# Optimization experiments

Measured on AMD Instinct MI355X. Metric: run time of the kernel, lower is better.

## Reference

```python
import jax, jax.numpy as jnp
import numpy as np

N_NODES, N_EDGES = 10000, 100000
NODE_DIM, NUM_BASIS = 128, 20
MULS = {0: 128, 1: 64, 2: 32}            # 128x0e + 64x1e + 32x2e
NUM_IRREPS = 224                          # total multiplicity count
HIDDEN = NODE_DIM + NUM_IRREPS            # 352
SPH_DIM = 128 * 1 + 64 * 3 + 32 * 5       # 480
LN_EPS = 1e-5

def _s2_basis():
    # orthonormal (Frobenius) basis of symmetric traceless 3x3 matrices (real l=2)
    s = np.zeros((5, 3, 3)); r2 = 1.0 / np.sqrt(2.0)
    s[0, 0, 1] = s[0, 1, 0] = r2
    s[1, 1, 2] = s[1, 2, 1] = r2
    s[2] = np.diag([-1.0, -1.0, 2.0]) / np.sqrt(6.0)
    s[3, 0, 2] = s[3, 2, 0] = r2
    s[4] = np.diag([1.0, -1.0, 0.0]) * r2
    return s

def _cg_tables():
    # real Clebsch-Gordan tensors for l<=2 built from the invariant tensors
    # delta, Levi-Civita, and the symmetric-traceless basis; unit Frobenius norm (e3nn w3j convention)
    e3 = np.zeros((3, 3, 3))
    e3[0, 1, 2] = e3[1, 2, 0] = e3[2, 0, 1] = 1.0
    e3[0, 2, 1] = e3[2, 1, 0] = e3[1, 0, 2] = -1.0
    S = _s2_basis(); I3 = np.eye(3); I5 = np.eye(5)
    nrm = lambda c: (c / np.linalg.norm(c)).astype(np.float32)
    cg = {(0, 0, 0): np.ones((1, 1, 1), np.float32)}
    cg[(0, 1, 1)] = nrm(I3[None]); cg[(1, 0, 1)] = nrm(I3[:, None, :]); cg[(1, 1, 0)] = nrm(I3[:, :, None])
    cg[(0, 2, 2)] = nrm(I5[None]); cg[(2, 0, 2)] = nrm(I5[:, None, :]); cg[(2, 2, 0)] = nrm(I5[:, :, None])
    cg[(1, 1, 1)] = nrm(e3)
    cg[(1, 1, 2)] = nrm(np.transpose(S, (1, 2, 0)))
    cg[(1, 2, 1)] = nrm(np.transpose(S, (1, 0, 2)))
    cg[(2, 1, 1)] = nrm(S)
    cg[(2, 2, 1)] = nrm(np.einsum('ijk,Mil,Nlj->MNk', e3, S, S))
    cg[(1, 2, 2)] = nrm(np.einsum('iab,Mac,Ncb->iMN', e3, S, S))
    cg[(2, 1, 2)] = nrm(np.einsum('jab,Mac,Ncb->MjN', e3, S, S))
    cg[(2, 2, 2)] = nrm(np.einsum('Mab,Nbc,Pca->MNP', S, S, S))
    return cg

CG = _cg_tables()
PATHS = [(0, 0, 0), (1, 1, 0), (2, 2, 0),
         (0, 1, 1), (1, 0, 1), (1, 1, 1), (1, 2, 1), (2, 1, 1), (2, 2, 1),
         (0, 2, 2), (1, 1, 2), (1, 2, 2), (2, 0, 2), (2, 1, 2), (2, 2, 2)]
FAN = {0: 224, 1: 384, 2: 352}   # e3nn 'element' path-norm fan-in per output irrep
TP_NUMW = sum(MULS[l1] * MULS[l3] for (l1, _, l3) in PATHS)

def _layernorm(x, w, b):
    mu = x.mean(-1, keepdims=True)
    var = ((x - mu) ** 2).mean(-1, keepdims=True)
    return (x - mu) * jax.lax.rsqrt(var + LN_EPS) * w + b

def _o3_layernorm(x, w, b):
    # equivariant layer norm: per-irrep RMS over (mul, m); mean-centering + bias only for scalars
    n = x.shape[0]; outs = []; off = 0; woff = 0
    for l in (0, 1, 2):
        mul, d = MULS[l], 2 * l + 1
        f = x[:, off:off + mul * d].reshape(n, mul, d)
        if l == 0:
            f = f - f.mean(axis=1, keepdims=True)
        nrm = (f * f).mean(axis=(1, 2), keepdims=True)
        f = f * jax.lax.rsqrt(nrm + LN_EPS) * w[woff:woff + mul][None, :, None]
        if l == 0:
            f = f + b[None, :, None]
        outs.append(f.reshape(n, mul * d)); off += mul * d; woff += mul
    return jnp.concatenate(outs, -1)

def _fc_tp(x1, x2, tp_w):
    # FullyConnectedTensorProduct(128x0e+64x1e+32x2e, 1x0e+1x1e+1x2e -> 128x0e+64x1e+32x2e)
    outs = {0: 0.0, 1: 0.0, 2: 0.0}; off = 0
    for (l1, l2, l3) in PATHS:
        m1, m3 = MULS[l1], MULS[l3]
        W = tp_w[off:off + m1 * m3].reshape(m1, m3); off += m1 * m3
        pw = float(np.sqrt((2 * l3 + 1) / FAN[l3]))
        outs[l3] = outs[l3] + pw * jnp.einsum('eum,en,mnk,uw->ewk', x1[l1], x2[l2], jnp.asarray(CG[(l1, l2, l3)]), W, optimize=True)
    e = x2[0].shape[0]
    return jnp.concatenate([outs[l].reshape(e, -1) for l in (0, 1, 2)], -1)

def _forward(x_scalar, x_spherical, rbf, rsh, ln_w, ln_b, o3_w, o3_b,
             mlp_w1, mlp_b1, mlp_w2, mlp_b2, rbf_w, tp_w, edge_index):
    scalar_in = _layernorm(x_scalar, ln_w, ln_b)                # [N,128]
    spherical_in = _o3_layernorm(x_spherical, o3_w, o3_b)       # [N,480]
    h = jax.nn.silu(scalar_in @ mlp_w1 + mlp_b1)
    scalar_out = h @ mlp_w2 + mlp_b2                            # [N,352]
    filt = rbf @ rbf_w                                          # [E,352]
    dst, src = edge_index[0], edge_index[1]
    fo = scalar_out[src] * filt                                 # gather + RBF filter
    gate, msg_scalar = fo[:, :NUM_IRREPS], fo[:, NUM_IRREPS:]
    sph = spherical_in[src]                                     # [E,480]
    e = sph.shape[0]
    # ElementwiseTensorProduct(edge_irreps, 224x0e): per-channel scalar gating
    x1 = {0: (sph[:, :128] * gate[:, :128])[:, :, None],
          1: sph[:, 128:320].reshape(e, 64, 3) * gate[:, 128:192, None],
          2: sph[:, 320:480].reshape(e, 32, 5) * gate[:, 192:224, None]}
    x2 = {0: rsh[:, :1], 1: rsh[:, 1:4], 2: rsh[:, 4:9]}
    msg_sph = _fc_tp(x1, x2, tp_w)                              # [E,480]
    new_scalar = scalar_in.at[dst].add(msg_scalar)
    new_spherical = spherical_in.at[dst].add(msg_sph)
    return new_scalar, new_spherical

def setup_inputs():
    key = jax.random.key(0)
    ks = jax.random.split(key, 9)
    return {
        'x_scalar': jax.random.normal(ks[0], (N_NODES, NODE_DIM), jnp.float32),
        'x_spherical': jax.random.normal(ks[1], (N_NODES, SPH_DIM), jnp.float32),
        'rbf': jax.random.uniform(ks[2], (N_EDGES, NUM_BASIS), jnp.float32),
        'rsh': jax.random.normal(ks[3], (N_EDGES, 9), jnp.float32),
        'edge_index': jax.random.randint(ks[4], (2, N_EDGES), 0, N_NODES, dtype=jnp.int32),
        'ln_w': jnp.ones((NODE_DIM,), jnp.float32),
        'ln_b': jnp.zeros((NODE_DIM,), jnp.float32),
        'o3_w': jnp.ones((NUM_IRREPS,), jnp.float32),
        'o3_b': jnp.zeros((128,), jnp.float32),
        'mlp_w1': jax.random.normal(ks[5], (NODE_DIM, NODE_DIM), jnp.float32) / np.sqrt(NODE_DIM),
        'mlp_b1': jnp.zeros((NODE_DIM,), jnp.float32),
        'mlp_w2': jax.random.normal(ks[6], (NODE_DIM, HIDDEN), jnp.float32) / np.sqrt(NODE_DIM),
        'mlp_b2': jnp.zeros((HIDDEN,), jnp.float32),
        'rbf_w': jax.random.normal(ks[7], (NUM_BASIS, HIDDEN), jnp.float32) / np.sqrt(NUM_BASIS),
        'tp_w': jax.random.normal(ks[8], (TP_NUMW,), jnp.float32),
    }

def reference(x_scalar, x_spherical, rbf, rsh, edge_index, ln_w, ln_b, o3_w, o3_b,
              mlp_w1, mlp_b1, mlp_w2, mlp_b2, rbf_w, tp_w):
    return _forward(x_scalar, x_spherical, rbf, rsh, ln_w, ln_b, o3_w, o3_b,
                    mlp_w1, mlp_b1, mlp_w2, mlp_b2, rbf_w, tp_w, edge_index)
```

## Files before the change

### kernel.cpp

```cpp
#include <hip/hip_runtime.h>

#define NN 10000
#define NE 100000
#define ND 128
#define NB 20
#define NIR 224
#define NH 352
#define SD 480
#define BS 512

#define CR   0.70710678118654752f
#define CA   0.40824829046386302f
#define HA   0.20412414523193151f
#define HR   0.35355339059327376f
#define C110 0.57735026918962576f
#define C220 0.44721359549995794f
#define C111 0.40824829046386302f
#define C11X 0.44721359549995794f
#define C221 0.36514837167011074f
#define C222 0.58554004376912270f
#define S32  0.86602540378443865f
#define PW0  0.066815310478106094f
#define PW1  0.088388347648318447f
#define PW2  0.11918321088232916f

typedef __bf16 v8bf __attribute__((ext_vector_type(8)));
typedef unsigned short us8v __attribute__((ext_vector_type(8)));
typedef float f32x4 __attribute__((ext_vector_type(4)));

__device__ __forceinline__ unsigned short f2bfc(float f) {
  __bf16 h = (__bf16)f;
  return __builtin_bit_cast(unsigned short, h);
}
__device__ __forceinline__ float bf2f(unsigned short h) {
  unsigned int u = ((unsigned int)h) << 16;
  return __builtin_bit_cast(float, u);
}

__device__ __forceinline__ float warpReduceSum(float v) {
  #pragma unroll
  for (int off = 32; off > 0; off >>= 1) v += __shfl_down(v, off, 64);
  return v;
}

__global__ __launch_bounds__(128) void node_ln_kernel(
    const float* __restrict__ xs, const float* __restrict__ xsph,
    const float* __restrict__ lnw, const float* __restrict__ lnb,
    const float* __restrict__ o3w, const float* __restrict__ o3b,
    float* __restrict__ s_in, float* __restrict__ sph_in,
    float* __restrict__ out0)
{
  const int n = blockIdx.x, t = threadIdx.x;
  __shared__ float red[4];

  auto reduce2 = [&](float a, float b) {
    a = warpReduceSum(a); b = warpReduceSum(b);
    if ((t & 63) == 0) { red[(t >> 6) * 2] = a; red[(t >> 6) * 2 + 1] = b; }
    __syncthreads();
    float ra = red[0] + red[2], rb = red[1] + red[3];
    __syncthreads();
    return make_float2(ra, rb);
  };

  float x = xs[n * ND + t];
  float2 sr = reduce2(x, x * x);
  float mu = sr.x * (1.f / ND);
  float var = sr.y * (1.f / ND) - mu * mu;
  float y = (x - mu) * rsqrtf(var + 1e-5f) * lnw[t] + lnb[t];
  s_in[n * ND + t] = y; out0[n * ND + t] = y;

  float f = xsph[n * SD + t];
  float2 r0 = reduce2(f, f * f);
  float m0 = r0.x * (1.f / 128.f);
  float nrm0 = r0.y * (1.f / 128.f) - m0 * m0;
  float y0 = (f - m0) * rsqrtf(nrm0 + 1e-5f) * o3w[t] + o3b[t];
  sph_in[n * SD + t] = y0;

  float f1a = xsph[n * SD + 128 + t];
  float f1b = (t < 64) ? xsph[n * SD + 256 + t] : 0.f;
  float2 r1 = reduce2(f1a * f1a + f1b * f1b, 0.f);
  float rs1 = rsqrtf(r1.x * (1.f / 192.f) + 1e-5f);
  sph_in[n * SD + 128 + t] = f1a * rs1 * o3w[128 + t / 3];
  if (t < 64)
    sph_in[n * SD + 256 + t] = f1b * rs1 * o3w[128 + (128 + t) / 3];

  float f2a = xsph[n * SD + 320 + t];
  float f2b = (t < 32) ? xsph[n * SD + 448 + t] : 0.f;
  float2 r2 = reduce2(f2a * f2a + f2b * f2b, 0.f);
  float rs2 = rsqrtf(r2.x * (1.f / 160.f) + 1e-5f);
  sph_in[n * SD + 320 + t] = f2a * rs2 * o3w[192 + t / 5];
  if (t < 32)
    sph_in[n * SD + 448 + t] = f2b * rs2 * o3w[192 + (128 + t) / 5];
}

#define NPB 8
__global__ __launch_bounds__(256) void mlp_kernel(
    const float* __restrict__ s_in, const float* __restrict__ w1,
    const float* __restrict__ b1, const float* __restrict__ w2,
    const float* __restrict__ b2, float* __restrict__ s_out)
{
  __shared__ float sIn[NPB][ND];
  __shared__ float sH[NPB][ND];
  const int t = threadIdx.x;
  const int n0 = blockIdx.x * NPB;
  for (int i = t; i < NPB * ND; i += 256) sIn[i >> 7][i & 127] = s_in[n0 * ND + i];
  __syncthreads();
  {
    const int j = t & 127, g = t >> 7;
    float acc[4] = {0.f, 0.f, 0.f, 0.f};
    for (int k = 0; k < ND; ++k) {
      float w = w1[k * ND + j];
      #pragma unroll
      for (int i = 0; i < 4; ++i) acc[i] = fmaf(sIn[g + 2 * i][k], w, acc[i]);
    }
    #pragma unroll
    for (int i = 0; i < 4; ++i) {
      float z = acc[i] + b1[j];
      sH[g + 2 * i][j] = z / (1.f + __expf(-z));
    }
  }
  __syncthreads();
  for (int jb = 0; jb < 2; ++jb) {
    int j = jb * 256 + t;
    if (j < NH) {
      float acc[NPB];
      #pragma unroll
      for (int i = 0; i < NPB; ++i) acc[i] = b2[j];
      for (int k = 0; k < ND; ++k) {
        float w = w2[k * NH + j];
        #pragma unroll
        for (int i = 0; i < NPB; ++i) acc[i] = fmaf(sH[i][k], w, acc[i]);
      }
      #pragma unroll
      for (int i = 0; i < NPB; ++i) s_out[(n0 + i) * NH + j] = acc[i];
    }
  }
}

__device__ __forceinline__ float wc0(const float* w, int u, int j) {
  int off = (u < 128) ? u * 128 : (u < 192) ? 16384 + (u - 128) * 128 : 24576 + (u - 192) * 128;
  return w[off + j];
}
__device__ __forceinline__ float wc1(const float* w, int u, int j) {
  int off = (u < 128) ? 28672 + u * 64 : (u < 192) ? 36864 + (u - 128) * 64
          : (u < 256) ? 40960 + (u - 192) * 64 : (u < 320) ? 45056 + (u - 256) * 64
          : (u < 352) ? 49152 + (u - 320) * 64 : 51200 + (u - 352) * 64;
  return w[off + j];
}
__device__ __forceinline__ float wc2(const float* w, int u, int j) {
  int off = (u < 128) ? 53248 + u * 32 : (u < 192) ? 57344 + (u - 128) * 32
          : (u < 256) ? 59392 + (u - 192) * 32 : (u < 288) ? 61440 + (u - 256) * 32
          : (u < 320) ? 62464 + (u - 288) * 32 : 63488 + (u - 320) * 32;
  return w[off + j];
}

__global__ __launch_bounds__(256) void prep_w_kernel(
    const float* __restrict__ tpw, const float* __restrict__ rbf_w,
    unsigned short* __restrict__ W0g, unsigned short* __restrict__ W1g,
    unsigned short* __restrict__ W2g, unsigned short* __restrict__ Wfq)
{
  int gid = blockIdx.x * 256 + threadIdx.x;
  int i = gid & 7, lane = (gid >> 3) & 63;
  int r = lane & 15, kl = lane >> 4;
  if (gid < 28672) {
    int fid = gid >> 9, kk = fid >> 3, wid = fid & 7;
    W0g[gid] = f2bfc(wc0(tpw, kk * 32 + kl * 8 + i, wid * 16 + r));
  } else if (gid < 53248) {
    int g = gid - 28672, fid = g >> 9, kk = fid >> 2, nt = fid & 3;
    W1g[g] = f2bfc(wc1(tpw, kk * 32 + kl * 8 + i, nt * 16 + r));
  } else if (gid < 65536) {
    int g = gid - 53248, fid = g >> 9, q = fid >> 2, kh = (fid >> 1) & 1, ntc = fid & 1;
    int kk = kh * 6 + q;
    W2g[g] = (kk < 11) ? f2bfc(wc2(tpw, kk * 32 + kl * 8 + i, ntc * 16 + r)) : (unsigned short)0;
  } else if (gid < 90112) {
    int g = gid - 65536, fid = g >> 9, q = fid >> 3, wid = fid & 7;
    int t44 = wid + q * 8, nt = t44 >> 1, k = kl * 8 + i;
    Wfq[g] = (t44 < 44 && k < 20) ? f2bfc(rbf_w[k * NH + nt * 16 + r]) : (unsigned short)0;
  }
}

template<int M>
__device__ __forceinline__ void emit_dot(unsigned short* dst, const unsigned short* x1,
                                         const int* offs, const float* cf) {
  us8v xv[M];
  #pragma unroll
  for (int m = 0; m < M; ++m) xv[m] = *(const us8v*)&x1[offs[m]];
  v8bf o;
  #pragma unroll
  for (int i = 0; i < 8; ++i) {
    float a = 0.f;
    #pragma unroll
    for (int m = 0; m < M; ++m) a = fmaf(cf[m], bf2f(xv[m][i]), a);
    o[i] = (__bf16)a;
  }
  *(us8v*)dst = __builtin_bit_cast(us8v, o);
}

#define TSW(e, idx) ((idx) ^ (((e) & 7) << 3))

__device__ __forceinline__ void build0(unsigned short* Tb, const unsigned short* X1u,
                                       const float* RshF, int tid) {
  for (int it = tid; it < 32 * 28; it += BS) {
    int e = it / 28, ub = it - e * 28, u0 = ub * 8;
    const float* R = &RshF[e * 9];
    const unsigned short* x1 = &X1u[e * 480];
    unsigned short* dst = Tb + TSW(e, e * 384 + u0);
    if (u0 < 128) {
      float cf[1] = { PW0 * R[0] };
      int offs[1] = { u0 };
      emit_dot<1>(dst, x1, offs, cf);
    } else if (u0 < 192) {
      int m0 = u0 - 128;
      float cf[3] = { PW0 * C110 * R[1], PW0 * C110 * R[2], PW0 * C110 * R[3] };
      int offs[3] = { 128 + m0, 192 + m0, 256 + m0 };
      emit_dot<3>(dst, x1, offs, cf);
    } else {
      int m0 = u0 - 192;
      float cf[5] = { PW0 * C220 * R[4], PW0 * C220 * R[5], PW0 * C220 * R[6],
                      PW0 * C220 * R[7], PW0 * C220 * R[8] };
      int offs[5] = { 320 + m0, 352 + m0, 384 + m0, 416 + m0, 448 + m0 };
      emit_dot<5>(dst, x1, offs, cf);
    }
  }
}

template<int k>
__device__ __forceinline__ void build1(unsigned short* Tb, const unsigned short* X1u,
                                       const float* RshF, int tid) {
  for (int it = tid; it < 32 * 48; it += BS) {
    int e = it / 48, ub = it - e * 48, u0 = ub * 8;
    const float* R = &RshF[e * 9];
    const unsigned short* x1 = &X1u[e * 480];
    unsigned short* dst = Tb + TSW(e, e * 384 + u0);
    const float s = R[0], v0 = R[1], v1 = R[2], v2 = R[3];
    const float w0 = R[4], w1 = R[5], w2 = R[6], w3 = R[7], w4 = R[8];
    if (u0 < 128) {
      float cf[1] = { PW1 * C110 * R[1 + k] };
      int offs[1] = { u0 };
      emit_dot<1>(dst, x1, offs, cf);
    } else if (u0 < 192) {
      float cf[1] = { PW1 * C110 * s };
      int offs[1] = { 128 + k * 64 + (u0 - 128) };
      emit_dot<1>(dst, x1, offs, cf);
    } else if (u0 < 256) {
      constexpr int ka = (k + 1) % 3, kb = (k + 2) % 3;
      int m0 = u0 - 192;
      float cf[2] = { PW1 * C111 * R[1 + kb], -PW1 * C111 * R[1 + ka] };
      int offs[2] = { 128 + ka * 64 + m0, 128 + kb * 64 + m0 };
      emit_dot<2>(dst, x1, offs, cf);
    } else if (u0 < 320) {
      int m0 = u0 - 256;
      float cf[3];
      if constexpr (k == 0) { cf[0] = PW1*C11X*(-CA*w2 + CR*w4); cf[1] = PW1*C11X*CR*w0; cf[2] = PW1*C11X*CR*w3; }
      else if constexpr (k == 1) { cf[0] = PW1*C11X*CR*w0; cf[1] = PW1*C11X*(-CA*w2 - CR*w4); cf[2] = PW1*C11X*CR*w1; }
      else { cf[0] = PW1*C11X*CR*w3; cf[1] = PW1*C11X*CR*w1; cf[2] = PW1*C11X*2.f*CA*w2; }
      int offs[3] = { 128 + m0, 192 + m0, 256 + m0 };
      emit_dot<3>(dst, x1, offs, cf);
    } else if (u0 < 352) {
      int m0 = u0 - 320;
      if constexpr (k == 0) {
        float cf[4] = { PW1*C11X*CR*v1, PW1*C11X*(-CA*v0), PW1*C11X*CR*v2, PW1*C11X*CR*v0 };
        int offs[4] = { 320 + m0, 384 + m0, 416 + m0, 448 + m0 };
        emit_dot<4>(dst, x1, offs, cf);
      } else if constexpr (k == 1) {
        float cf[4] = { PW1*C11X*CR*v0, PW1*C11X*CR*v2, PW1*C11X*(-CA*v1), PW1*C11X*(-CR*v1) };
        int offs[4] = { 320 + m0, 352 + m0, 384 + m0, 448 + m0 };
        emit_dot<4>(dst, x1, offs, cf);
      } else {
        float cf[3] = { PW1*C11X*CR*v1, PW1*C11X*2.f*CA*v2, PW1*C11X*CR*v0 };
        int offs[3] = { 352 + m0, 384 + m0, 416 + m0 };
        emit_dot<3>(dst, x1, offs, cf);
      }
    } else {
      int m0 = u0 - 352;
      if constexpr (k == 0) {
        float cf[5] = { PW1*C221*0.5f*w3, PW1*C221*(S32*w2 + 0.5f*w4), PW1*C221*(-S32*w1),
                        PW1*C221*(-0.5f*w0), PW1*C221*(-0.5f*w1) };
        int offs[5] = { 320 + m0, 352 + m0, 384 + m0, 416 + m0, 448 + m0 };
        emit_dot<5>(dst, x1, offs, cf);
      } else if constexpr (k == 1) {
        float cf[5] = { PW1*C221*(-0.5f*w1), PW1*C221*0.5f*w0, PW1*C221*S32*w3,
                        PW1*C221*(-S32*w2 + 0.5f*w4), PW1*C221*(-0.5f*w3) };
        int offs[5] = { 320 + m0, 352 + m0, 384 + m0, 416 + m0, 448 + m0 };
        emit_dot<5>(dst, x1, offs, cf);
      } else {
        float cf[4] = { PW1*C221*(-w4), PW1*C221*(-0.5f*w3), PW1*C221*0.5f*w1, PW1*C221*w0 };
        int offs[4] = { 320 + m0, 352 + m0, 416 + m0, 448 + m0 };
        emit_dot<4>(dst, x1, offs, cf);
      }
    }
  }
}

template<int K>
__device__ __forceinline__ void build2(unsigned short* Tb, const unsigned short* X1u,
                                       const float* RshF, int tid) {
  for (int it = tid; it < 32 * 44; it += BS) {
    int e = it / 44, ub = it - e * 44, u0 = ub * 8;
    const float* R = &RshF[e * 9];
    const unsigned short* x1 = &X1u[e * 480];
    unsigned short* dst = Tb + TSW(e, e * 384 + u0);
    const float s = R[0], v0 = R[1], v1 = R[2], v2 = R[3];
    const float w0 = R[4], w1 = R[5], w2 = R[6], w3 = R[7], w4 = R[8];
    if (u0 < 128) {
      float cf[1] = { PW2 * C220 * R[4 + K] };
      int offs[1] = { u0 };
      emit_dot<1>(dst, x1, offs, cf);
    } else if (u0 < 192) {
      int m0 = u0 - 128;
      if constexpr (K == 0) {
        float cf[2] = { PW2*C11X*CR*v1, PW2*C11X*CR*v0 };
        int offs[2] = { 128 + m0, 192 + m0 };
        emit_dot<2>(dst, x1, offs, cf);
      } else if constexpr (K == 1) {
        float cf[2] = { PW2*C11X*CR*v2, PW2*C11X*CR*v1 };
        int offs[2] = { 192 + m0, 256 + m0 };
        emit_dot<2>(dst, x1, offs, cf);
      } else if constexpr (K == 2) {
        float cf[3] = { PW2*C11X*(-CA*v0), PW2*C11X*(-CA*v1), PW2*C11X*2.f*CA*v2 };
        int offs[3] = { 128 + m0, 192 + m0, 256 + m0 };
        emit_dot<3>(dst, x1, offs, cf);
      } else if constexpr (K == 3) {
        float cf[2] = { PW2*C11X*CR*v2, PW2*C11X*CR*v0 };
        int offs[2] = { 128 + m0, 256 + m0 };
        emit_dot<2>(dst, x1, offs, cf);
      } else {
        float cf[2] = { PW2*C11X*CR*v0, PW2*C11X*(-CR*v1) };
        int offs[2] = { 128 + m0, 192 + m0 };
        emit_dot<2>(dst, x1, offs, cf);
      }
    } else if (u0 < 256) {
      int m0 = u0 - 192;
      if constexpr (K == 2) {
        float cf[2] = { PW2*C221*S32*w1, PW2*C221*(-S32*w3) };
        int offs[2] = { 128 + m0, 192 + m0 };
        emit_dot<2>(dst, x1, offs, cf);
      } else {
        float cf[3];
        if constexpr (K == 0) { cf[0]=PW2*C221*(-0.5f*w3); cf[1]=PW2*C221*0.5f*w1; cf[2]=PW2*C221*w4; }
        else if constexpr (K == 1) { cf[0]=PW2*C221*(-S32*w2 - 0.5f*w4); cf[1]=PW2*C221*(-0.5f*w0); cf[2]=PW2*C221*0.5f*w3; }
        else if constexpr (K == 3) { cf[0]=PW2*C221*0.5f*w0; cf[1]=PW2*C221*(S32*w2 - 0.5f*w4); cf[2]=PW2*C221*(-0.5f*w1); }
        else { cf[0]=PW2*C221*0.5f*w1; cf[1]=PW2*C221*0.5f*w3; cf[2]=PW2*C221*(-w0); }
        int offs[3] = { 128 + m0, 192 + m0, 256 + m0 };
        emit_dot<3>(dst, x1, offs, cf);
      }
    } else if (u0 < 288) {
      int m0 = u0 - 256;
      float cf[1] = { PW2 * C220 * s };
      int offs[1] = { 320 + K * 32 + m0 };
      emit_dot<1>(dst, x1, offs, cf);
    } else if (u0 < 320) {
      int m0 = u0 - 288;
      if constexpr (K == 0) {
        float cf[3] = { PW2*C221*0.5f*v1, PW2*C221*(-0.5f*v0), PW2*C221*v2 };
        int offs[3] = { 352 + m0, 416 + m0, 448 + m0 };
        emit_dot<3>(dst, x1, offs, cf);
      } else if constexpr (K == 1) {
        float cf[4] = { PW2*C221*(-0.5f*v1), PW2*C221*(-S32*v0), PW2*C221*0.5f*v2, PW2*C221*(-0.5f*v0) };
        int offs[4] = { 320 + m0, 384 + m0, 416 + m0, 448 + m0 };
        emit_dot<4>(dst, x1, offs, cf);
      } else if constexpr (K == 2) {
        float cf[2] = { PW2*C221*S32*v0, PW2*C221*(-S32*v1) };
        int offs[2] = { 352 + m0, 416 + m0 };
        emit_dot<2>(dst, x1, offs, cf);
      } else if constexpr (K == 3) {
        float cf[4] = { PW2*C221*0.5f*v0, PW2*C221*(-0.5f*v2), PW2*C221*S32*v1, PW2*C221*(-0.5f*v1) };
        int offs[4] = { 320 + m0, 352 + m0, 384 + m0, 448 + m0 };
        emit_dot<4>(dst, x1, offs, cf);
      } else {
        float cf[3] = { PW2*C221*(-v2), PW2*C221*0.5f*v0, PW2*C221*0.5f*v1 };
        int offs[3] = { 320 + m0, 352 + m0, 416 + m0 };
        emit_dot<3>(dst, x1, offs, cf);
      }
    } else {
      int m0 = u0 - 320;
      if constexpr (K == 0) {
        float cf[4] = { PW2*C222*(-CA*w2), PW2*C222*HR*w3, PW2*C222*(-CA*w0), PW2*C222*HR*w1 };
        int offs[4] = { 320 + m0, 352 + m0, 384 + m0, 416 + m0 };
        emit_dot<4>(dst, x1, offs, cf);
      } else if constexpr (K == 4) {
        float cf[4] = { PW2*C222*(-HR*w1), PW2*C222*(-CA*w4), PW2*C222*HR*w3, PW2*C222*(-CA*w2) };
        int offs[4] = { 352 + m0, 384 + m0, 416 + m0, 448 + m0 };
        emit_dot<4>(dst, x1, offs, cf);
      } else {
        float cf[5];
        if constexpr (K == 1) { cf[0]=PW2*C222*HR*w3; cf[1]=PW2*C222*(HA*w2 - HR*w4); cf[2]=PW2*C222*HA*w1; cf[3]=PW2*C222*HR*w0; cf[4]=PW2*C222*(-HR*w1); }
        else if constexpr (K == 2) { cf[0]=PW2*C222*(-CA*w0); cf[1]=PW2*C222*HA*w1; cf[2]=PW2*C222*CA*w2; cf[3]=PW2*C222*HA*w3; cf[4]=PW2*C222*(-CA*w4); }
        else { cf[0]=PW2*C222*HR*w1; cf[1]=PW2*C222*HR*w0; cf[2]=PW2*C222*HA*w3; cf[3]=PW2*C222*(HA*w2 + HR*w4); cf[4]=PW2*C222*HR*w3; }
        int offs[5] = { 320 + m0, 352 + m0, 384 + m0, 416 + m0, 448 + m0 };
        emit_dot<5>(dst, x1, offs, cf);
      }
    }
  }
}

__global__ __launch_bounds__(BS, 4) void tp_fused_kernel(
    const float* __restrict__ rbf, const float* __restrict__ rsh,
    const int* __restrict__ ei, const float* __restrict__ s_out,
    const float* __restrict__ sph_in,
    const unsigned short* __restrict__ W0g, const unsigned short* __restrict__ W1g,
    const unsigned short* __restrict__ W2g, const unsigned short* __restrict__ Wfq,
    float* __restrict__ out0, float* __restrict__ out1T)
{
  __shared__ __align__(16) unsigned char smem[81280];
  unsigned short* Tb0 = (unsigned short*)smem;
  unsigned short* Tb1 = (unsigned short*)(smem + 24576);
  unsigned short* gateU = (unsigned short*)smem;
  unsigned short* rbfpadU = (unsigned short*)(smem + 24576);
  unsigned short* X1u = (unsigned short*)(smem + 49152);
  float* RshF = (float*)(smem + 79872);
  int* EdstS = (int*)(smem + 81024);
  int* EsrcS = (int*)(smem + 81152);

  const int tid = threadIdx.x;
  const int wid = tid >> 6, lane = tid & 63;
  const int r = lane & 15, kl = lane >> 4;

  auto MFMA = [](v8bf a, v8bf b, f32x4 c) {
    return __builtin_amdgcn_mfma_f32_16x16x32_bf16(a, b, c, 0, 0, 0);
  };
  auto ldw = [&](const unsigned short* base, int fid) {
    return __builtin_bit_cast(v8bf, *(const us8v*)&base[fid * 512 + lane * 8]);
  };

  auto mfma_l0 = [&](const unsigned short* T) {
    f32x4 acc0 = {0.f, 0.f, 0.f, 0.f}, acc1 = {0.f, 0.f, 0.f, 0.f};
    #pragma unroll
    for (int kk = 0; kk < 7; ++kk) {
      v8bf b = ldw(W0g, kk * 8 + wid);
      us8v a0 = *(const us8v*)&T[TSW(r, r * 384 + kl * 8 + kk * 32)];
      us8v a1 = *(const us8v*)&T[TSW(r, (16 + r) * 384 + kl * 8 + kk * 32)];
      acc0 = MFMA(__builtin_bit_cast(v8bf, a0), b, acc0);
      acc1 = MFMA(__builtin_bit_cast(v8bf, a1), b, acc1);
    }
    int col = wid * 16 + r;
    #pragma unroll
    for (int j = 0; j < 4; ++j) {
      unsafeAtomicAdd(&out1T[(long)EdstS[kl * 4 + j] * SD + col], acc0[j]);
      unsafeAtomicAdd(&out1T[(long)EdstS[16 + kl * 4 + j] * SD + col], acc1[j]);
    }
  };

  auto mfma_l1 = [&](const unsigned short* T, int k) {
    const int mt = wid >> 2, nt = wid & 3;
    f32x4 acc = {0.f, 0.f, 0.f, 0.f};
    #pragma unroll
    for (int kk = 0; kk < 12; ++kk) {
      v8bf b = ldw(W1g, kk * 4 + nt);
      us8v a = *(const us8v*)&T[TSW(r, (mt * 16 + r) * 384 + kl * 8 + kk * 32)];
      acc = MFMA(__builtin_bit_cast(v8bf, a), b, acc);
    }
    int col = 128 + k * 64 + nt * 16 + r;
    #pragma unroll
    for (int j = 0; j < 4; ++j)
      unsafeAtomicAdd(&out1T[(long)EdstS[mt * 16 + kl * 4 + j] * SD + col], acc[j]);
  };

  auto mfma_l2 = [&](const unsigned short* T, int K) {
    const int kh = wid >> 2, mt = (wid >> 1) & 1, ntc = wid & 1;
    f32x4 acc = {0.f, 0.f, 0.f, 0.f};
    #pragma unroll
    for (int q = 0; q < 6; ++q) {
      if (kh == 0 || q < 5) {
        v8bf b = ldw(W2g, q * 4 + kh * 2 + ntc);
        us8v a = *(const us8v*)&T[TSW(r, (mt * 16 + r) * 384 + kh * 192 + q * 32 + kl * 8)];
        acc = MFMA(__builtin_bit_cast(v8bf, a), b, acc);
      }
    }
    int col = 320 + K * 32 + ntc * 16 + r;
    #pragma unroll
    for (int j = 0; j < 4; ++j)
      unsafeAtomicAdd(&out1T[(long)EdstS[mt * 16 + kl * 4 + j] * SD + col], acc[j]);
  };

  for (int tile = blockIdx.x; tile < NE / 32; tile += gridDim.x) {
    const int e0 = tile * 32;
    for (int i = tid; i < 32; i += BS) { EdstS[i] = ei[e0 + i]; EsrcS[i] = ei[NE + e0 + i]; }
    for (int i = tid; i < 288; i += BS) RshF[i] = rsh[(long)e0 * 9 + i];
    for (int i = tid; i < 1024; i += BS) {
      int e = i >> 5, b = i & 31;
      rbfpadU[e * 40 + b] = (b < 20) ? f2bfc(rbf[(long)(e0 + e) * NB + b]) : (unsigned short)0;
    }
    __syncthreads();
    {
      us8v ra0 = *(const us8v*)&rbfpadU[r * 40 + kl * 8];
      us8v ra1 = *(const us8v*)&rbfpadU[(16 + r) * 40 + kl * 8];
      v8bf av0 = __builtin_bit_cast(v8bf, ra0);
      v8bf av1 = __builtin_bit_cast(v8bf, ra1);
      #pragma unroll
      for (int q = 0; q < 6; ++q) {
        int t44 = wid + q * 8;
        if (t44 < 44) {
          int mt = t44 & 1, nt = t44 >> 1;
          v8bf b = ldw(Wfq, q * 8 + wid);
          f32x4 acc = {0.f, 0.f, 0.f, 0.f};
          acc = MFMA(mt ? av1 : av0, b, acc);
          int gi = nt * 16 + r;
          #pragma unroll
          for (int j = 0; j < 4; ++j) {
            int e = mt * 16 + kl * 4 + j;
            float so = s_out[(long)EsrcS[e] * NH + gi];
            float val = acc[j] * so;
            if (nt < 14) gateU[e * 232 + gi] = f2bfc(val);
            else unsafeAtomicAdd(&out0[(long)EdstS[e] * ND + (gi - 224)], val);
          }
        }
      }
    }
    __syncthreads();
    for (int it = tid; it < 1920; it += BS) {
      int e = it / 60, cb = it - e * 60, c0 = cb * 8;
      long srow = (long)EsrcS[e] * SD;
      v8bf o;
      if (c0 < 128) {
        us8v gv = *(const us8v*)&gateU[e * 232 + c0];
        const float4 sa = *(const float4*)&sph_in[srow + c0];
        const float4 sb = *(const float4*)&sph_in[srow + c0 + 4];
        float sv[8] = {sa.x, sa.y, sa.z, sa.w, sb.x, sb.y, sb.z, sb.w};
        #pragma unroll
        for (int i = 0; i < 8; ++i) o[i] = (__bf16)(sv[i] * bf2f(gv[i]));
      } else if (c0 < 320) {
        int m = (c0 - 128) >> 6, mul0 = (c0 - 128) & 63;
        us8v gv = *(const us8v*)&gateU[e * 232 + 128 + mul0];
        #pragma unroll
        for (int i = 0; i < 8; ++i)
          o[i] = (__bf16)(sph_in[srow + 128 + (mul0 + i) * 3 + m] * bf2f(gv[i]));
      } else {
        int m = (c0 - 320) >> 5, mul0 = (c0 - 320) & 31;
        us8v gv = *(const us8v*)&gateU[e * 232 + 192 + mul0];
        #pragma unroll
        for (int i = 0; i < 8; ++i)
          o[i] = (__bf16)(sph_in[srow + 320 + (mul0 + i) * 5 + m] * bf2f(gv[i]));
      }
      *(us8v*)&X1u[e * 480 + c0] = __builtin_bit_cast(us8v, o);
    }
    __syncthreads();
    build0(Tb0, X1u, RshF, tid); __syncthreads();
    build1<0>(Tb1, X1u, RshF, tid); mfma_l0(Tb0); __syncthreads();
    build1<1>(Tb0, X1u, RshF, tid); mfma_l1(Tb1, 0); __syncthreads();
    build1<2>(Tb1, X1u, RshF, tid); mfma_l1(Tb0, 1); __syncthreads();
    build2<0>(Tb0, X1u, RshF, tid); mfma_l1(Tb1, 2); __syncthreads();
    build2<1>(Tb1, X1u, RshF, tid); mfma_l2(Tb0, 0); __syncthreads();
    build2<2>(Tb0, X1u, RshF, tid); mfma_l2(Tb1, 1); __syncthreads();
    build2<3>(Tb1, X1u, RshF, tid); mfma_l2(Tb0, 2); __syncthreads();
    build2<4>(Tb0, X1u, RshF, tid); mfma_l2(Tb1, 3); __syncthreads();
    mfma_l2(Tb0, 4); __syncthreads();
  }
}

__global__ __launch_bounds__(512) void merge_kernel(
    const float* __restrict__ sph_in, const float* __restrict__ out1T,
    float* __restrict__ out1)
{
  const int n = blockIdx.x, t = threadIdx.x;
  if (t < SD) {
    int tT;
    if (t < 128) tT = t;
    else if (t < 320) { int c = t - 128; int mul = c / 3, k = c - mul * 3; tT = 128 + k * 64 + mul; }
    else { int c = t - 320; int mul = c / 5, K = c - mul * 5; tT = 320 + K * 32 + mul; }
    out1[(long)n * SD + t] = sph_in[(long)n * SD + t] + out1T[(long)n * SD + tT];
  }
}

extern "C" void kernel_launch(void* const* d_in, const int* in_sizes, int n_in,
                              void* d_out, int out_size, void* d_ws, size_t ws_size,
                              hipStream_t stream)
{
  const float* xs   = (const float*)d_in[0];
  const float* xsph = (const float*)d_in[1];
  const float* rbf  = (const float*)d_in[2];
  const float* rsh  = (const float*)d_in[3];
  const int*   ei   = (const int*)d_in[4];
  const float* lnw  = (const float*)d_in[5];
  const float* lnb  = (const float*)d_in[6];
  const float* o3w  = (const float*)d_in[7];
  const float* o3b  = (const float*)d_in[8];
  const float* w1   = (const float*)d_in[9];
  const float* b1   = (const float*)d_in[10];
  const float* w2   = (const float*)d_in[11];
  const float* b2   = (const float*)d_in[12];
  const float* rbfw = (const float*)d_in[13];
  const float* tpw  = (const float*)d_in[14];

  float* out0 = (float*)d_out;
  float* out1 = out0 + (size_t)NN * ND;

  float* ws      = (float*)d_ws;
  float* s_in    = ws;
  float* sph_in  = ws + (size_t)NN * ND;
  float* s_out   = ws + (size_t)NN * (ND + SD);
  float* out1T   = ws + (size_t)NN * (ND + SD + NH);
  unsigned short* wbase = (unsigned short*)(ws + (size_t)NN * (ND + 2 * SD + NH));
  unsigned short* W0g = wbase;
  unsigned short* W1g = wbase + 28672;
  unsigned short* W2g = wbase + 53248;
  unsigned short* Wfq = wbase + 65536;

  hipMemsetAsync(out1T, 0, (size_t)NN * SD * sizeof(float), stream);
  prep_w_kernel<<<352, 256, 0, stream>>>(tpw, rbfw, W0g, W1g, W2g, Wfq);
  node_ln_kernel<<<NN, 128, 0, stream>>>(xs, xsph, lnw, lnb, o3w, o3b, s_in, sph_in, out0);
  mlp_kernel<<<NN / NPB, 256, 0, stream>>>(s_in, w1, b1, w2, b2, s_out);
  tp_fused_kernel<<<512, BS, 0, stream>>>(rbf, rsh, ei, s_out, sph_in,
                                          W0g, W1g, W2g, Wfq, out0, out1T);
  merge_kernel<<<NN, 512, 0, stream>>>(sph_in, out1T, out1);
}
```

Before: 645.1 us.

## Store normalized spherical features in transposed layout and batch atomic scatters

The node layernorm kernel now writes the spherical features in the m-major (transposed) layout the tensor-product kernel consumes. The per-edge gather therefore becomes two contiguous float4 loads instead of strided scalar loads. The atomic scatter of MFMA results into out1T is deferred and grouped into two batches after the l0/l1 and l2 stages, with accumulators held in registers. This cuts per-stage atomic epilogues and branch divergence, at the cost of more live accumulator registers under a launch bound of 4 blocks.

```diff
diff --git a/kernel.cpp b/kernel.cpp
--- a/kernel.cpp
+++ b/kernel.cpp
@@ -43,11 +43,17 @@
   return v;
 }
 
+__device__ __forceinline__ int t2tT(int t) {
+  if (t < 128) return t;
+  if (t < 320) { int c = t - 128; return 128 + (c % 3) * 64 + c / 3; }
+  int c = t - 320; return 320 + (c % 5) * 32 + c / 5;
+}
+
 __global__ __launch_bounds__(128) void node_ln_kernel(
     const float* __restrict__ xs, const float* __restrict__ xsph,
     const float* __restrict__ lnw, const float* __restrict__ lnb,
     const float* __restrict__ o3w, const float* __restrict__ o3b,
-    float* __restrict__ s_in, float* __restrict__ sph_in,
+    float* __restrict__ s_in, float* __restrict__ sphT,
     float* __restrict__ out0)
 {
   const int n = blockIdx.x, t = threadIdx.x;
@@ -74,23 +80,23 @@
   float m0 = r0.x * (1.f / 128.f);
   float nrm0 = r0.y * (1.f / 128.f) - m0 * m0;
   float y0 = (f - m0) * rsqrtf(nrm0 + 1e-5f) * o3w[t] + o3b[t];
-  sph_in[n * SD + t] = y0;
+  sphT[n * SD + t] = y0;
 
   float f1a = xsph[n * SD + 128 + t];
   float f1b = (t < 64) ? xsph[n * SD + 256 + t] : 0.f;
   float2 r1 = reduce2(f1a * f1a + f1b * f1b, 0.f);
   float rs1 = rsqrtf(r1.x * (1.f / 192.f) + 1e-5f);
-  sph_in[n * SD + 128 + t] = f1a * rs1 * o3w[128 + t / 3];
+  sphT[n * SD + t2tT(128 + t)] = f1a * rs1 * o3w[128 + t / 3];
   if (t < 64)
-    sph_in[n * SD + 256 + t] = f1b * rs1 * o3w[128 + (128 + t) / 3];
+    sphT[n * SD + t2tT(256 + t)] = f1b * rs1 * o3w[128 + (128 + t) / 3];
 
   float f2a = xsph[n * SD + 320 + t];
   float f2b = (t < 32) ? xsph[n * SD + 448 + t] : 0.f;
   float2 r2 = reduce2(f2a * f2a + f2b * f2b, 0.f);
   float rs2 = rsqrtf(r2.x * (1.f / 160.f) + 1e-5f);
-  sph_in[n * SD + 320 + t] = f2a * rs2 * o3w[192 + t / 5];
+  sphT[n * SD + t2tT(320 + t)] = f2a * rs2 * o3w[192 + t / 5];
   if (t < 32)
-    sph_in[n * SD + 448 + t] = f2b * rs2 * o3w[192 + (128 + t) / 5];
+    sphT[n * SD + t2tT(448 + t)] = f2b * rs2 * o3w[192 + (128 + t) / 5];
 }
 
 #define NPB 8
@@ -397,7 +403,7 @@
 __global__ __launch_bounds__(BS, 4) void tp_fused_kernel(
     const float* __restrict__ rbf, const float* __restrict__ rsh,
     const int* __restrict__ ei, const float* __restrict__ s_out,
-    const float* __restrict__ sph_in,
+    const float* __restrict__ sphT,
     const unsigned short* __restrict__ W0g, const unsigned short* __restrict__ W1g,
     const unsigned short* __restrict__ W2g, const unsigned short* __restrict__ Wfq,
     float* __restrict__ out0, float* __restrict__ out1T)
@@ -423,8 +429,7 @@
     return __builtin_bit_cast(v8bf, *(const us8v*)&base[fid * 512 + lane * 8]);
   };
 
-  auto mfma_l0 = [&](const unsigned short* T) {
-    f32x4 acc0 = {0.f, 0.f, 0.f, 0.f}, acc1 = {0.f, 0.f, 0.f, 0.f};
+  auto mfma_l0 = [&](const unsigned short* T, f32x4& acc0, f32x4& acc1) {
     #pragma unroll
     for (int kk = 0; kk < 7; ++kk) {
       v8bf b = ldw(W0g, kk * 8 + wid);
@@ -433,32 +438,20 @@
       acc0 = MFMA(__builtin_bit_cast(v8bf, a0), b, acc0);
       acc1 = MFMA(__builtin_bit_cast(v8bf, a1), b, acc1);
     }
-    int col = wid * 16 + r;
-    #pragma unroll
-    for (int j = 0; j < 4; ++j) {
-      unsafeAtomicAdd(&out1T[(long)EdstS[kl * 4 + j] * SD + col], acc0[j]);
-      unsafeAtomicAdd(&out1T[(long)EdstS[16 + kl * 4 + j] * SD + col], acc1[j]);
-    }
   };
 
-  auto mfma_l1 = [&](const unsigned short* T, int k) {
+  auto mfma_l1 = [&](const unsigned short* T, f32x4& acc) {
     const int mt = wid >> 2, nt = wid & 3;
-    f32x4 acc = {0.f, 0.f, 0.f, 0.f};
     #pragma unroll
     for (int kk = 0; kk < 12; ++kk) {
       v8bf b = ldw(W1g, kk * 4 + nt);
       us8v a = *(const us8v*)&T[TSW(r, (mt * 16 + r) * 384 + kl * 8 + kk * 32)];
       acc = MFMA(__builtin_bit_cast(v8bf, a), b, acc);
     }
-    int col = 128 + k * 64 + nt * 16 + r;
-    #pragma unroll
-    for (int j = 0; j < 4; ++j)
-      unsafeAtomicAdd(&out1T[(long)EdstS[mt * 16 + kl * 4 + j] * SD + col], acc[j]);
   };
 
-  auto mfma_l2 = [&](const unsigned short* T, int K) {
+  auto mfma_l2 = [&](const unsigned short* T, f32x4& acc) {
     const int kh = wid >> 2, mt = (wid >> 1) & 1, ntc = wid & 1;
-    f32x4 acc = {0.f, 0.f, 0.f, 0.f};
     #pragma unroll
     for (int q = 0; q < 6; ++q) {
       if (kh == 0 || q < 5) {
@@ -467,10 +460,6 @@
         acc = MFMA(__builtin_bit_cast(v8bf, a), b, acc);
       }
     }
-    int col = 320 + K * 32 + ntc * 16 + r;
-    #pragma unroll
-    for (int j = 0; j < 4; ++j)
-      unsafeAtomicAdd(&out1T[(long)EdstS[mt * 16 + kl * 4 + j] * SD + col], acc[j]);
   };
 
   for (int tile = blockIdx.x; tile < NE / 32; tile += gridDim.x) {
@@ -511,54 +500,73 @@
     for (int it = tid; it < 1920; it += BS) {
       int e = it / 60, cb = it - e * 60, c0 = cb * 8;
       long srow = (long)EsrcS[e] * SD;
+      int gidx = (c0 < 128) ? c0 : (c0 < 320) ? 128 + (c0 & 63) : 192 + (c0 & 31);
+      us8v gv = *(const us8v*)&gateU[e * 232 + gidx];
+      const float4 sa = *(const float4*)&sphT[srow + c0];
+      const float4 sb = *(const float4*)&sphT[srow + c0 + 4];
+      float sv[8] = {sa.x, sa.y, sa.z, sa.w, sb.x, sb.y, sb.z, sb.w};
       v8bf o;
-      if (c0 < 128) {
-        us8v gv = *(const us8v*)&gateU[e * 232 + c0];
-        const float4 sa = *(const float4*)&sph_in[srow + c0];
-        const float4 sb = *(const float4*)&sph_in[srow + c0 + 4];
-        float sv[8] = {sa.x, sa.y, sa.z, sa.w, sb.x, sb.y, sb.z, sb.w};
-        #pragma unroll
-        for (int i = 0; i < 8; ++i) o[i] = (__bf16)(sv[i] * bf2f(gv[i]));
-      } else if (c0 < 320) {
-        int m = (c0 - 128) >> 6, mul0 = (c0 - 128) & 63;
-        us8v gv = *(const us8v*)&gateU[e * 232 + 128 + mul0];
-        #pragma unroll
-        for (int i = 0; i < 8; ++i)
-          o[i] = (__bf16)(sph_in[srow + 128 + (mul0 + i) * 3 + m] * bf2f(gv[i]));
-      } else {
-        int m = (c0 - 320) >> 5, mul0 = (c0 - 320) & 31;
-        us8v gv = *(const us8v*)&gateU[e * 232 + 192 + mul0];
-        #pragma unroll
-        for (int i = 0; i < 8; ++i)
-          o[i] = (__bf16)(sph_in[srow + 320 + (mul0 + i) * 5 + m] * bf2f(gv[i]));
-      }
+      #pragma unroll
+      for (int i = 0; i < 8; ++i) o[i] = (__bf16)(sv[i] * bf2f(gv[i]));
       *(us8v*)&X1u[e * 480 + c0] = __builtin_bit_cast(us8v, o);
     }
     __syncthreads();
+
+    f32x4 z = {0.f, 0.f, 0.f, 0.f};
+    f32x4 aL0a = z, aL0b = z;
+    f32x4 aL1_0 = z, aL1_1 = z, aL1_2 = z;
+    f32x4 aL2_0 = z, aL2_1 = z, aL2_2 = z, aL2_3 = z, aL2_4 = z;
+
     build0(Tb0, X1u, RshF, tid); __syncthreads();
-    build1<0>(Tb1, X1u, RshF, tid); mfma_l0(Tb0); __syncthreads();
-    build1<1>(Tb0, X1u, RshF, tid); mfma_l1(Tb1, 0); __syncthreads();
-    build1<2>(Tb1, X1u, RshF, tid); mfma_l1(Tb0, 1); __syncthreads();
-    build2<0>(Tb0, X1u, RshF, tid); mfma_l1(Tb1, 2); __syncthreads();
-    build2<1>(Tb1, X1u, RshF, tid); mfma_l2(Tb0, 0); __syncthreads();
-    build2<2>(Tb0, X1u, RshF, tid); mfma_l2(Tb1, 1); __syncthreads();
-    build2<3>(Tb1, X1u, RshF, tid); mfma_l2(Tb0, 2); __syncthreads();
-    build2<4>(Tb0, X1u, RshF, tid); mfma_l2(Tb1, 3); __syncthreads();
-    mfma_l2(Tb0, 4); __syncthreads();
+    build1<0>(Tb1, X1u, RshF, tid); mfma_l0(Tb0, aL0a, aL0b); __syncthreads();
+    build1<1>(Tb0, X1u, RshF, tid); mfma_l1(Tb1, aL1_0); __syncthreads();
+    build1<2>(Tb1, X1u, RshF, tid); mfma_l1(Tb0, aL1_1); __syncthreads();
+    build2<0>(Tb0, X1u, RshF, tid); mfma_l1(Tb1, aL1_2);
+    {
+      int col0 = wid * 16 + r;
+      const int mt = wid >> 2, nt = wid & 3;
+      int col1 = 128 + nt * 16 + r;
+      #pragma unroll
+      for (int j = 0; j < 4; ++j) {
+        unsafeAtomicAdd(&out1T[(long)EdstS[kl * 4 + j] * SD + col0], aL0a[j]);
+        unsafeAtomicAdd(&out1T[(long)EdstS[16 + kl * 4 + j] * SD + col0], aL0b[j]);
+        long rowb = (long)EdstS[mt * 16 + kl * 4 + j] * SD;
+        unsafeAtomicAdd(&out1T[rowb + col1], aL1_0[j]);
+        unsafeAtomicAdd(&out1T[rowb + col1 + 64], aL1_1[j]);
+        unsafeAtomicAdd(&out1T[rowb + col1 + 128], aL1_2[j]);
+      }
+    }
+    __syncthreads();
+    build2<1>(Tb1, X1u, RshF, tid); mfma_l2(Tb0, aL2_0); __syncthreads();
+    build2<2>(Tb0, X1u, RshF, tid); mfma_l2(Tb1, aL2_1); __syncthreads();
+    build2<3>(Tb1, X1u, RshF, tid); mfma_l2(Tb0, aL2_2); __syncthreads();
+    build2<4>(Tb0, X1u, RshF, tid); mfma_l2(Tb1, aL2_3); __syncthreads();
+    mfma_l2(Tb0, aL2_4);
+    {
+      const int mt = (wid >> 1) & 1, ntc = wid & 1;
+      int col2 = 320 + ntc * 16 + r;
+      #pragma unroll
+      for (int j = 0; j < 4; ++j) {
+        long rowb = (long)EdstS[mt * 16 + kl * 4 + j] * SD;
+        unsafeAtomicAdd(&out1T[rowb + col2], aL2_0[j]);
+        unsafeAtomicAdd(&out1T[rowb + col2 + 32], aL2_1[j]);
+        unsafeAtomicAdd(&out1T[rowb + col2 + 64], aL2_2[j]);
+        unsafeAtomicAdd(&out1T[rowb + col2 + 96], aL2_3[j]);
+        unsafeAtomicAdd(&out1T[rowb + col2 + 128], aL2_4[j]);
+      }
+    }
+    __syncthreads();
   }
 }
 
 __global__ __launch_bounds__(512) void merge_kernel(
-    const float* __restrict__ sph_in, const float* __restrict__ out1T,
+    const float* __restrict__ sphT, const float* __restrict__ out1T,
     float* __restrict__ out1)
 {
   const int n = blockIdx.x, t = threadIdx.x;
   if (t < SD) {
-    int tT;
-    if (t < 128) tT = t;
-    else if (t < 320) { int c = t - 128; int mul = c / 3, k = c - mul * 3; tT = 128 + k * 64 + mul; }
-    else { int c = t - 320; int mul = c / 5, K = c - mul * 5; tT = 320 + K * 32 + mul; }
-    out1[(long)n * SD + t] = sph_in[(long)n * SD + t] + out1T[(long)n * SD + tT];
+    int tT = t2tT(t);
+    out1[(long)n * SD + t] = sphT[(long)n * SD + tT] + out1T[(long)n * SD + tT];
   }
 }
 
@@ -587,7 +595,7 @@
 
   float* ws      = (float*)d_ws;
   float* s_in    = ws;
-  float* sph_in  = ws + (size_t)NN * ND;
+  float* sphT    = ws + (size_t)NN * ND;
   float* s_out   = ws + (size_t)NN * (ND + SD);
   float* out1T   = ws + (size_t)NN * (ND + SD + NH);
   unsigned short* wbase = (unsigned short*)(ws + (size_t)NN * (ND + 2 * SD + NH));
@@ -598,9 +606,9 @@
 
   hipMemsetAsync(out1T, 0, (size_t)NN * SD * sizeof(float), stream);
   prep_w_kernel<<<352, 256, 0, stream>>>(tpw, rbfw, W0g, W1g, W2g, Wfq);
-  node_ln_kernel<<<NN, 128, 0, stream>>>(xs, xsph, lnw, lnb, o3w, o3b, s_in, sph_in, out0);
+  node_ln_kernel<<<NN, 128, 0, stream>>>(xs, xsph, lnw, lnb, o3w, o3b, s_in, sphT, out0);
   mlp_kernel<<<NN / NPB, 256, 0, stream>>>(s_in, w1, b1, w2, b2, s_out);
-  tp_fused_kernel<<<512, BS, 0, stream>>>(rbf, rsh, ei, s_out, sph_in,
+  tp_fused_kernel<<<512, BS, 0, stream>>>(rbf, rsh, ei, s_out, sphT,
                                           W0g, W1g, W2g, Wfq, out0, out1T);
-  merge_kernel<<<NN, 512, 0, stream>>>(sph_in, out1T, out1);
-}
+  merge_kernel<<<NN, 512, 0, stream>>>(sphT, out1T, out1);
+}
```

Result: slower. 718.9 us (+11.4%).

## Sort edges by destination and store spherical features in transposed component-major layout

Applied to the files above, without the earlier changes.

Adds a counting sort (histogram, scan, scatter) that reorders edges by destination node. Each tile of the fused tensor-product kernel then has clustered destinations, which should improve locality for the atomic scatter into out1T. The normalized spherical features are now written in the same component-major (transposed) layout the kernel consumes, so the gather becomes two contiguous float4 loads instead of strided scalar loads. The cost is three extra small kernels and a memset, plus indirect reads of rbf and rsh through the sorted edge id, which lose coalescing.

```diff
diff --git a/kernel.cpp b/kernel.cpp
--- a/kernel.cpp
+++ b/kernel.cpp
@@ -43,11 +43,49 @@
   return v;
 }
 
+__device__ __forceinline__ int t2tT(int t) {
+  if (t < 128) return t;
+  if (t < 320) { int c = t - 128; return 128 + (c % 3) * 64 + c / 3; }
+  int c = t - 320; return 320 + (c % 5) * 32 + c / 5;
+}
+
+__global__ __launch_bounds__(256) void sort_hist(const int* __restrict__ ei, int* __restrict__ cnt) {
+  int e = blockIdx.x * 256 + threadIdx.x;
+  if (e < NE) atomicAdd(&cnt[ei[e]], 1);
+}
+
+__global__ __launch_bounds__(1024) void sort_scan(const int* __restrict__ cnt, int* __restrict__ cursor) {
+  __shared__ int part[1024];
+  const int t = threadIdx.x;
+  int loc[10]; int s = 0;
+  #pragma unroll
+  for (int j = 0; j < 10; ++j) { int idx = t * 10 + j; int v = (idx < NN) ? cnt[idx] : 0; loc[j] = s; s += v; }
+  part[t] = s; __syncthreads();
+  for (int d = 1; d < 1024; d <<= 1) {
+    int v = (t >= d) ? part[t - d] : 0; __syncthreads();
+    part[t] += v; __syncthreads();
+  }
+  int off = part[t] - s;
+  #pragma unroll
+  for (int j = 0; j < 10; ++j) { int idx = t * 10 + j; if (idx < NN) cursor[idx] = off + loc[j]; }
+}
+
+__global__ __launch_bounds__(256) void sort_scatter(
+    const int* __restrict__ ei, int* __restrict__ cursor,
+    int* __restrict__ es_dst, int* __restrict__ es_src, int* __restrict__ es_eid) {
+  int e = blockIdx.x * 256 + threadIdx.x;
+  if (e < NE) {
+    int d = ei[e];
+    int pos = atomicAdd(&cursor[d], 1);
+    es_dst[pos] = d; es_src[pos] = ei[NE + e]; es_eid[pos] = e;
+  }
+}
+
 __global__ __launch_bounds__(128) void node_ln_kernel(
     const float* __restrict__ xs, const float* __restrict__ xsph,
     const float* __restrict__ lnw, const float* __restrict__ lnb,
     const float* __restrict__ o3w, const float* __restrict__ o3b,
-    float* __restrict__ s_in, float* __restrict__ sph_in,
+    float* __restrict__ s_in, float* __restrict__ sphT,
     float* __restrict__ out0)
 {
   const int n = blockIdx.x, t = threadIdx.x;
@@ -74,23 +112,23 @@
   float m0 = r0.x * (1.f / 128.f);
   float nrm0 = r0.y * (1.f / 128.f) - m0 * m0;
   float y0 = (f - m0) * rsqrtf(nrm0 + 1e-5f) * o3w[t] + o3b[t];
-  sph_in[n * SD + t] = y0;
+  sphT[n * SD + t] = y0;
 
   float f1a = xsph[n * SD + 128 + t];
   float f1b = (t < 64) ? xsph[n * SD + 256 + t] : 0.f;
   float2 r1 = reduce2(f1a * f1a + f1b * f1b, 0.f);
   float rs1 = rsqrtf(r1.x * (1.f / 192.f) + 1e-5f);
-  sph_in[n * SD + 128 + t] = f1a * rs1 * o3w[128 + t / 3];
+  sphT[n * SD + t2tT(128 + t)] = f1a * rs1 * o3w[128 + t / 3];
   if (t < 64)
-    sph_in[n * SD + 256 + t] = f1b * rs1 * o3w[128 + (128 + t) / 3];
+    sphT[n * SD + t2tT(256 + t)] = f1b * rs1 * o3w[128 + (128 + t) / 3];
 
   float f2a = xsph[n * SD + 320 + t];
   float f2b = (t < 32) ? xsph[n * SD + 448 + t] : 0.f;
   float2 r2 = reduce2(f2a * f2a + f2b * f2b, 0.f);
   float rs2 = rsqrtf(r2.x * (1.f / 160.f) + 1e-5f);
-  sph_in[n * SD + 320 + t] = f2a * rs2 * o3w[192 + t / 5];
+  sphT[n * SD + t2tT(320 + t)] = f2a * rs2 * o3w[192 + t / 5];
   if (t < 32)
-    sph_in[n * SD + 448 + t] = f2b * rs2 * o3w[192 + (128 + t) / 5];
+    sphT[n * SD + t2tT(448 + t)] = f2b * rs2 * o3w[192 + (128 + t) / 5];
 }
 
 #define NPB 8
@@ -396,13 +434,14 @@
 
 __global__ __launch_bounds__(BS, 4) void tp_fused_kernel(
     const float* __restrict__ rbf, const float* __restrict__ rsh,
-    const int* __restrict__ ei, const float* __restrict__ s_out,
-    const float* __restrict__ sph_in,
+    const int* __restrict__ es_dst, const int* __restrict__ es_src,
+    const int* __restrict__ es_eid,
+    const float* __restrict__ s_out, const float* __restrict__ sphT,
     const unsigned short* __restrict__ W0g, const unsigned short* __restrict__ W1g,
     const unsigned short* __restrict__ W2g, const unsigned short* __restrict__ Wfq,
     float* __restrict__ out0, float* __restrict__ out1T)
 {
-  __shared__ __align__(16) unsigned char smem[81280];
+  __shared__ __align__(16) unsigned char smem[81408];
   unsigned short* Tb0 = (unsigned short*)smem;
   unsigned short* Tb1 = (unsigned short*)(smem + 24576);
   unsigned short* gateU = (unsigned short*)smem;
@@ -411,6 +450,7 @@
   float* RshF = (float*)(smem + 79872);
   int* EdstS = (int*)(smem + 81024);
   int* EsrcS = (int*)(smem + 81152);
+  int* EidS  = (int*)(smem + 81280);
 
   const int tid = threadIdx.x;
   const int wid = tid >> 6, lane = tid & 63;
@@ -475,11 +515,14 @@
 
   for (int tile = blockIdx.x; tile < NE / 32; tile += gridDim.x) {
     const int e0 = tile * 32;
-    for (int i = tid; i < 32; i += BS) { EdstS[i] = ei[e0 + i]; EsrcS[i] = ei[NE + e0 + i]; }
-    for (int i = tid; i < 288; i += BS) RshF[i] = rsh[(long)e0 * 9 + i];
+    for (int i = tid; i < 32; i += BS) {
+      EdstS[i] = es_dst[e0 + i]; EsrcS[i] = es_src[e0 + i]; EidS[i] = es_eid[e0 + i];
+    }
+    __syncthreads();
+    for (int i = tid; i < 288; i += BS) RshF[i] = rsh[(long)EidS[i / 9] * 9 + i % 9];
     for (int i = tid; i < 1024; i += BS) {
       int e = i >> 5, b = i & 31;
-      rbfpadU[e * 40 + b] = (b < 20) ? f2bfc(rbf[(long)(e0 + e) * NB + b]) : (unsigned short)0;
+      rbfpadU[e * 40 + b] = (b < 20) ? f2bfc(rbf[(long)EidS[e] * NB + b]) : (unsigned short)0;
     }
     __syncthreads();
     {
@@ -511,27 +554,14 @@
     for (int it = tid; it < 1920; it += BS) {
       int e = it / 60, cb = it - e * 60, c0 = cb * 8;
       long srow = (long)EsrcS[e] * SD;
+      int gidx = (c0 < 128) ? c0 : (c0 < 320) ? 128 + (c0 & 63) : 192 + (c0 & 31);
+      us8v gv = *(const us8v*)&gateU[e * 232 + gidx];
+      const float4 sa = *(const float4*)&sphT[srow + c0];
+      const float4 sb = *(const float4*)&sphT[srow + c0 + 4];
+      float sv[8] = {sa.x, sa.y, sa.z, sa.w, sb.x, sb.y, sb.z, sb.w};
       v8bf o;
-      if (c0 < 128) {
-        us8v gv = *(const us8v*)&gateU[e * 232 + c0];
-        const float4 sa = *(const float4*)&sph_in[srow + c0];
-        const float4 sb = *(const float4*)&sph_in[srow + c0 + 4];
-        float sv[8] = {sa.x, sa.y, sa.z, sa.w, sb.x, sb.y, sb.z, sb.w};
-        #pragma unroll
-        for (int i = 0; i < 8; ++i) o[i] = (__bf16)(sv[i] * bf2f(gv[i]));
-      } else if (c0 < 320) {
-        int m = (c0 - 128) >> 6, mul0 = (c0 - 128) & 63;
-        us8v gv = *(const us8v*)&gateU[e * 232 + 128 + mul0];
-        #pragma unroll
-        for (int i = 0; i < 8; ++i)
-          o[i] = (__bf16)(sph_in[srow + 128 + (mul0 + i) * 3 + m] * bf2f(gv[i]));
-      } else {
-        int m = (c0 - 320) >> 5, mul0 = (c0 - 320) & 31;
-        us8v gv = *(const us8v*)&gateU[e * 232 + 192 + mul0];
-        #pragma unroll
-        for (int i = 0; i < 8; ++i)
-          o[i] = (__bf16)(sph_in[srow + 320 + (mul0 + i) * 5 + m] * bf2f(gv[i]));
-      }
+      #pragma unroll
+      for (int i = 0; i < 8; ++i) o[i] = (__bf16)(sv[i] * bf2f(gv[i]));
       *(us8v*)&X1u[e * 480 + c0] = __builtin_bit_cast(us8v, o);
     }
     __syncthreads();
@@ -549,16 +579,13 @@
 }
 
 __global__ __launch_bounds__(512) void merge_kernel(
-    const float* __restrict__ sph_in, const float* __restrict__ out1T,
+    const float* __restrict__ sphT, const float* __restrict__ out1T,
     float* __restrict__ out1)
 {
   const int n = blockIdx.x, t = threadIdx.x;
   if (t < SD) {
-    int tT;
-    if (t < 128) tT = t;
-    else if (t < 320) { int c = t - 128; int mul = c / 3, k = c - mul * 3; tT = 128 + k * 64 + mul; }
-    else { int c = t - 320; int mul = c / 5, K = c - mul * 5; tT = 320 + K * 32 + mul; }
-    out1[(long)n * SD + t] = sph_in[(long)n * SD + t] + out1T[(long)n * SD + tT];
+    int tT = t2tT(t);
+    out1[(long)n * SD + t] = sphT[(long)n * SD + tT] + out1T[(long)n * SD + tT];
   }
 }
 
@@ -587,7 +614,7 @@
 
   float* ws      = (float*)d_ws;
   float* s_in    = ws;
-  float* sph_in  = ws + (size_t)NN * ND;
+  float* sphT    = ws + (size_t)NN * ND;
   float* s_out   = ws + (size_t)NN * (ND + SD);
   float* out1T   = ws + (size_t)NN * (ND + SD + NH);
   unsigned short* wbase = (unsigned short*)(ws + (size_t)NN * (ND + 2 * SD + NH));
@@ -595,12 +622,22 @@
   unsigned short* W1g = wbase + 28672;
   unsigned short* W2g = wbase + 53248;
   unsigned short* Wfq = wbase + 65536;
+  int* ibase  = (int*)(wbase + 90112);
+  int* cnt    = ibase;
+  int* cursor = ibase + 10000;
+  int* es_dst = ibase + 20000;
+  int* es_src = ibase + 120000;
+  int* es_eid = ibase + 220000;
 
   hipMemsetAsync(out1T, 0, (size_t)NN * SD * sizeof(float), stream);
+  hipMemsetAsync(cnt, 0, (size_t)NN * sizeof(int), stream);
+  sort_hist<<<(NE + 255) / 256, 256, 0, stream>>>(ei, cnt);
+  sort_scan<<<1, 1024, 0, stream>>>(cnt, cursor);
+  sort_scatter<<<(NE + 255) / 256, 256, 0, stream>>>(ei, cursor, es_dst, es_src, es_eid);
   prep_w_kernel<<<352, 256, 0, stream>>>(tpw, rbfw, W0g, W1g, W2g, Wfq);
-  node_ln_kernel<<<NN, 128, 0, stream>>>(xs, xsph, lnw, lnb, o3w, o3b, s_in, sph_in, out0);
+  node_ln_kernel<<<NN, 128, 0, stream>>>(xs, xsph, lnw, lnb, o3w, o3b, s_in, sphT, out0);
   mlp_kernel<<<NN / NPB, 256, 0, stream>>>(s_in, w1, b1, w2, b2, s_out);
-  tp_fused_kernel<<<512, BS, 0, stream>>>(rbf, rsh, ei, s_out, sph_in,
+  tp_fused_kernel<<<512, BS, 0, stream>>>(rbf, rsh, es_dst, es_src, es_eid, s_out, sphT,
                                           W0g, W1g, W2g, Wfq, out0, out1T);
-  merge_kernel<<<NN, 512, 0, stream>>>(sph_in, out1T, out1);
-}
+  merge_kernel<<<NN, 512, 0, stream>>>(sphT, out1T, out1);
+}
```

Measured after the change: 1.041 ms. 1.61x slower.
